# Kernel tuning notes

Hardware: AMD Instinct MI355X
Metric: run time of the kernel (lower is better)

## Reference

```python
import jax, jax.numpy as jnp
import numpy as np
import math

H = 16          # n_head
N_EMBD = 1024
EPS = 1e-5      # torch LayerNorm default


def setup_inputs() -> dict:
    key = jax.random.key(0)
    ks = jax.random.split(key, 6)
    B, T, C = 2, 2048, 1024
    x = jax.random.normal(ks[0], (B, T, C), dtype=jnp.float32)
    s = 0.02  # GPT-2 style init scale keeps softmax logits sane
    Wq = jax.random.normal(ks[1], (C, N_EMBD), dtype=jnp.float32) * s
    Wk = jax.random.normal(ks[2], (C, N_EMBD), dtype=jnp.float32) * s
    Wv = jax.random.normal(ks[3], (C, N_EMBD), dtype=jnp.float32) * s
    Wo = jax.random.normal(ks[4], (N_EMBD, C), dtype=jnp.float32) * s
    return {
        "x": x,
        "Wq": Wq, "bq": jnp.zeros((N_EMBD,), jnp.float32),
        "Wk": Wk, "bk": jnp.zeros((N_EMBD,), jnp.float32),
        "Wv": Wv, "bv": jnp.zeros((N_EMBD,), jnp.float32),
        "Wo": Wo, "bo": jnp.zeros((C,), jnp.float32),
        "gamma": jnp.ones((C,), jnp.float32),
        "beta": jnp.zeros((C,), jnp.float32),
    }


def reference(x, Wq, bq, Wk, bk, Wv, bv, Wo, bo, gamma, beta):
    B, T, _ = x.shape
    Dh = N_EMBD // H
    # projections -> (B, H, T, Dh)
    def split_heads(y):
        return y.reshape(B, T, H, Dh).transpose(0, 2, 1, 3)
    q = split_heads(x @ Wq + bq)
    k = split_heads(x @ Wk + bk)
    v = split_heads(x @ Wv + bv)
    # naive causal attention: explicit (B,H,T,T) scores
    att = jnp.einsum("bhtd,bhsd->bhts", q, k) * (1.0 / math.sqrt(Dh))
    causal = jnp.tril(jnp.ones((T, T), dtype=bool))
    att = jnp.where(causal[None, None], att, -jnp.inf)
    att = jax.nn.softmax(att, axis=-1)
    o = jnp.einsum("bhts,bhsd->bhtd", att, v)
    o = o.transpose(0, 2, 1, 3).reshape(B, T, N_EMBD)
    y = o @ Wo + bo
    # LayerNorm (dropout is identity at p=0 / eval)
    mu = jnp.mean(y, axis=-1, keepdims=True)
    var = jnp.var(y, axis=-1, keepdims=True)
    return (y - mu) * jax.lax.rsqrt(var + EPS) * gamma + beta
```

## Files before the change

### kernel.cpp

```cpp
#include <hip/hip_runtime.h>
#include <stdint.h>
#include <stddef.h>

typedef __attribute__((ext_vector_type(8))) short short8;
typedef __attribute__((ext_vector_type(4))) float f32x4;
typedef __attribute__((ext_vector_type(16))) float f32x16;
typedef __attribute__((ext_vector_type(4))) unsigned short us4;
typedef __attribute__((ext_vector_type(4))) unsigned u32x4;

#define DEVI static __device__ __forceinline__

DEVI unsigned short f2bf(float f) {
  unsigned u = __builtin_bit_cast(unsigned, f);
  u += 0x7FFFu + ((u >> 16) & 1u);
  return (unsigned short)(u >> 16);
}

DEVI float bf2f(unsigned short u) {
  return __builtin_bit_cast(float, ((unsigned)u) << 16);
}

DEVI f32x4 mfma16(short8 a, short8 b, f32x4 c) {
  return __builtin_amdgcn_mfma_f32_16x16x32_bf16(a, b, c, 0, 0, 0);
}

DEVI f32x16 mfma32(short8 a, short8 b, f32x16 c) {
  return __builtin_amdgcn_mfma_f32_32x32x16_bf16(a, b, c, 0, 0, 0);
}

DEVI unsigned cvtpk(float lo, float hi) {
  unsigned r;
  asm("v_cvt_pk_bf16_f32 %0, %1, %2" : "=v"(r) : "v"(lo), "v"(hi));
  return r;
}

DEVI void plswap(unsigned& a, unsigned& b) {
  asm("v_permlane32_swap_b32 %0, %1" : "+v"(a), "+v"(b));
}

DEVI float ex2(float x) {
  float r;
  asm("v_exp_f32 %0, %1" : "=v"(r) : "v"(x));
  return r;
}

DEVI f32x16 zero16() {
  f32x16 z;
#pragma unroll
  for (int i = 0; i < 16; ++i) z[i] = 0.f;
  return z;
}

DEVI void glds16(const void* g, void* l) {
  __builtin_amdgcn_global_load_lds(
      (const __attribute__((address_space(1))) void*)g,
      (__attribute__((address_space(3))) void*)l, 16, 0, 0);
}

__global__ __launch_bounds__(256) void k_prep(const float* __restrict__ x,
                                              unsigned short* __restrict__ xb,
                                              const float* __restrict__ W0,
                                              const float* __restrict__ W1,
                                              const float* __restrict__ W2,
                                              const float* __restrict__ W3,
                                              unsigned short* __restrict__ WT) {
  __shared__ float tile[64][65];
  const int b = blockIdx.x;
  if (b < 2048) {
    size_t i = ((size_t)b * 256 + threadIdx.x) * 8;
    f32x4 a = *(const f32x4*)(x + i);
    f32x4 v2 = *(const f32x4*)(x + i + 4);
    short8 v;
#pragma unroll
    for (int j = 0; j < 4; ++j) {
      v[j] = (short)f2bf(a[j]);
      v[4 + j] = (short)f2bf(v2[j]);
    }
    *(short8*)(xb + i) = v;
    return;
  }
  const int lin = b - 2048;
  const int z = lin >> 8, rem = lin & 255;
  const float* W = (z == 0) ? W0 : (z == 1) ? W1 : (z == 2) ? W2 : W3;
  unsigned short* out = WT + (size_t)z * 1024 * 1024;
  const int n0 = (rem & 15) * 64, k0 = (rem >> 4) * 64;
  const int t = threadIdx.x, rr = t >> 4, cc = (t & 15) * 4;
#pragma unroll
  for (int i = 0; i < 4; ++i) {
    int row = i * 16 + rr;
    f32x4 v = *(const f32x4*)(W + (size_t)(k0 + row) * 1024 + n0 + cc);
#pragma unroll
    for (int j = 0; j < 4; ++j) tile[row][cc + j] = v[j];
  }
  __syncthreads();
#pragma unroll
  for (int i = 0; i < 4; ++i) {
    int nrow = i * 16 + rr;
    us4 u;
#pragma unroll
    for (int j = 0; j < 4; ++j) u[j] = f2bf(tile[cc + j][nrow]);
    *(us4*)(out + (size_t)(n0 + nrow) * 1024 + k0 + cc) = u;
  }
}

template <bool SWAP>
DEVI void gemm_core2(const unsigned short* __restrict__ A,
                     const unsigned short* __restrict__ Bt,
                     int mt, int nt, char* lds, f32x4 (&acc)[4][4]) {
  const int t = threadIdx.x;
  const int l = t & 63, c = l & 15, g = l >> 4;
  const int w = t >> 6, wr = w >> 1, wc = w & 1;
  const int srow = t >> 3;
  const int sxor = (((t & 7) ^ (srow & 7))) * 8;
  const unsigned short* Ab = A + (size_t)(mt * 128 + srow) * 1024 + sxor;
  const unsigned short* Bb = Bt + (size_t)(nt * 128 + srow) * 1024 + sxor;
  const int key = (c & 7);

  auto STAGE = [&](int kt, int buf) {
    char* lb = lds + buf * 32768;
#pragma unroll
    for (int i = 0; i < 4; ++i) {
      glds16(Ab + (size_t)i * 32 * 1024 + kt * 64, lb + i * 4096 + t * 16);
      glds16(Bb + (size_t)i * 32 * 1024 + kt * 64, lb + 16384 + i * 4096 + t * 16);
    }
  };

  STAGE(0, 0);
  asm volatile("s_waitcnt vmcnt(0)" ::: "memory");
  __builtin_amdgcn_s_barrier();
  asm volatile("" ::: "memory");
  for (int kt = 0; kt < 16; ++kt) {
    const int cur = kt & 1;
    if (kt < 15) STAGE(kt + 1, cur ^ 1);
    const char* lb = lds + cur * 32768;
#pragma unroll
    for (int ks = 0; ks < 2; ++ks) {
      short8 af[4], bfr[4];
#pragma unroll
      for (int m = 0; m < 4; ++m)
        af[m] = *(const short8*)(lb + (wr * 64 + m * 16 + c) * 128 +
                                 ((ks * 4 + g) ^ key) * 16);
#pragma unroll
      for (int n = 0; n < 4; ++n)
        bfr[n] = *(const short8*)(lb + 16384 + (wc * 64 + n * 16 + c) * 128 +
                                  ((ks * 4 + g) ^ key) * 16);
#pragma unroll
      for (int m = 0; m < 4; ++m)
#pragma unroll
        for (int n = 0; n < 4; ++n)
          acc[m][n] = SWAP ? mfma16(bfr[n], af[m], acc[m][n])
                           : mfma16(af[m], bfr[n], acc[m][n]);
    }
    asm volatile("s_waitcnt vmcnt(0)" ::: "memory");
    __builtin_amdgcn_s_barrier();
    asm volatile("" ::: "memory");
  }
}

DEVI void gemm_core5(const unsigned short* __restrict__ A,
                     const unsigned short* __restrict__ Bt,
                     int mt, int pt, char* lds, f32x4 (&acc)[8][3]) {
  const int t = threadIdx.x;
  const int l = t & 63, c = l & 15, g = l >> 4;
  const int w = t >> 6, wm = w >> 2, wn = w & 3;
  const int srow = t >> 3;
  const int sxor = ((t & 7) ^ (srow & 7)) * 8;
  const unsigned short* Ab = A + (size_t)(mt * 256 + srow) * 1024 + sxor;
  const unsigned short* Bb = Bt + (size_t)(pt * 192 + srow) * 1024 + sxor;
  const int key = c & 7;

  auto STAGE = [&](int kt, int buf) {
    char* lb = lds + buf * 57344;
#pragma unroll
    for (int i = 0; i < 4; ++i)
      glds16(Ab + (size_t)(i * 64) * 1024 + kt * 64, lb + i * 8192 + t * 16);
#pragma unroll
    for (int i = 0; i < 3; ++i)
      glds16(Bb + (size_t)(i * 64) * 1024 + kt * 64, lb + 32768 + i * 8192 + t * 16);
  };

  STAGE(0, 0);
  asm volatile("s_waitcnt vmcnt(0)" ::: "memory");
  __builtin_amdgcn_s_barrier();
  asm volatile("" ::: "memory");
  for (int kt = 0; kt < 16; ++kt) {
    const int cur = kt & 1;
    if (kt < 15) STAGE(kt + 1, cur ^ 1);
    const char* la = lds + cur * 57344;
    const char* lbB = la + 32768;
    short8 bf[3][2];
#pragma unroll
    for (int fc = 0; fc < 3; ++fc)
#pragma unroll
      for (int ks = 0; ks < 2; ++ks) {
        int brow = wn * 48 + fc * 16 + c;
        bf[fc][ks] = *(const short8*)(lbB + brow * 128 + (((ks * 4 + g) ^ key) * 16));
      }
#pragma unroll
    for (int p = 0; p < 4; ++p) {
      short8 af[2][2];
#pragma unroll
      for (int r2 = 0; r2 < 2; ++r2)
#pragma unroll
        for (int ks = 0; ks < 2; ++ks) {
          int arow = wm * 128 + (2 * p + r2) * 16 + c;
          af[r2][ks] = *(const short8*)(la + arow * 128 + (((ks * 4 + g) ^ key) * 16));
        }
      __builtin_amdgcn_s_setprio(1);
#pragma unroll
      for (int ks = 0; ks < 2; ++ks)
#pragma unroll
        for (int r2 = 0; r2 < 2; ++r2)
#pragma unroll
          for (int fc = 0; fc < 3; ++fc)
            acc[2 * p + r2][fc] = mfma16(bf[fc][ks], af[r2][ks], acc[2 * p + r2][fc]);
      __builtin_amdgcn_s_setprio(0);
    }
    asm volatile("s_waitcnt vmcnt(0)" ::: "memory");
    __builtin_amdgcn_s_barrier();
    asm volatile("" ::: "memory");
  }
}

__global__ __launch_bounds__(512) void k_gemm_qkv3(
    const unsigned short* __restrict__ A,
    const unsigned short* __restrict__ Wf,
    const float* __restrict__ b0, const float* __restrict__ b1, const float* __restrict__ b2,
    unsigned short* __restrict__ O0, unsigned short* __restrict__ O1,
    unsigned short* __restrict__ O2) {
  extern __shared__ char lds[];
  const int mt = blockIdx.x, pt = blockIdx.y;
  f32x4 acc[8][3];
#pragma unroll
  for (int m = 0; m < 8; ++m)
#pragma unroll
    for (int n = 0; n < 3; ++n) acc[m][n] = (f32x4){0.f, 0.f, 0.f, 0.f};
  gemm_core5(A, Wf, mt, pt, lds, acc);
  const int t = threadIdx.x, l = t & 63, c = l & 15, g = l >> 4;
  const int w = t >> 6, wm = w >> 2, wn = w & 3;
#pragma unroll
  for (int fc = 0; fc < 3; ++fc) {
    int colg3 = pt * 192 + wn * 48 + fc * 16 + 4 * g;
    int z = colg3 >> 10, colc = colg3 & 1023;
    const float* bias = (z == 0) ? b0 : (z == 1) ? b1 : b2;
    f32x4 bv4 = *(const f32x4*)(bias + colc);
    int h = colc >> 6, d = colc & 63;
    if (z < 2) {
      unsigned short* out = (z == 0) ? O0 : O1;
      const float sc = (z == 0) ? 0.18033688011f : 1.0f;
#pragma unroll
      for (int fr = 0; fr < 8; ++fr) {
        int rowg = mt * 256 + wm * 128 + fr * 16 + c;
        int b = rowg >> 11, tt = rowg & 2047;
        us4 u;
#pragma unroll
        for (int r = 0; r < 4; ++r) u[r] = f2bf((acc[fr][fc][r] + bv4[r]) * sc);
        *(us4*)(out + ((size_t)(b * 16 + h) * 2048 + tt) * 64 + d) = u;
      }
    } else {
#pragma unroll
      for (int fr = 0; fr < 8; ++fr) {
        int rowg = mt * 256 + wm * 128 + fr * 16 + c;
        int b = rowg >> 11, tt = rowg & 2047;
        size_t base = ((size_t)(b * 16 + h) * 64 + d) * 2048 + tt;
#pragma unroll
        for (int r = 0; r < 4; ++r)
          O2[base + (size_t)r * 2048] = f2bf(acc[fr][fc][r] + bv4[r]);
      }
    }
  }
}

__global__ __launch_bounds__(256) void k_gemm_proj(const unsigned short* __restrict__ A,
                                                   const unsigned short* __restrict__ Bt,
                                                   const float* __restrict__ bias,
                                                   unsigned short* __restrict__ Yb) {
  __shared__ char lds[65536];
  f32x4 acc[4][4];
#pragma unroll
  for (int m = 0; m < 4; ++m)
#pragma unroll
    for (int n = 0; n < 4; ++n) acc[m][n] = (f32x4){0.f, 0.f, 0.f, 0.f};
  const int lin = blockIdx.y * 32 + blockIdx.x;
  const int nt = lin & 7, mt = lin >> 3;
  gemm_core2<true>(A, Bt, mt, nt, lds, acc);
  const int t = threadIdx.x, l = t & 63, c = l & 15, g = l >> 4;
  const int w = t >> 6, wr = w >> 1, wc = w & 1;
#pragma unroll
  for (int n = 0; n < 4; ++n) {
    int colb = nt * 128 + wc * 64 + n * 16 + 4 * g;
    f32x4 bv4 = *(const f32x4*)(bias + colb);
#pragma unroll
    for (int m = 0; m < 4; ++m) {
      int rowg = mt * 128 + wr * 64 + m * 16 + c;
      us4 u;
#pragma unroll
      for (int r = 0; r < 4; ++r) u[r] = f2bf(acc[m][n][r] + bv4[r]);
      *(us4*)(Yb + (size_t)rowg * 1024 + colb) = u;
    }
  }
}

__global__ __launch_bounds__(256) void k_attn11(const unsigned short* __restrict__ Q,
                                                const unsigned short* __restrict__ K,
                                                const unsigned short* __restrict__ VT,
                                                unsigned short* __restrict__ O,
                                                unsigned short* __restrict__ P,
                                                float* __restrict__ L) {
  __shared__ char lds[32768];
  const int bid = blockIdx.x;
  int qt, c0, NT, mode, bh, ci = 0;
  if (bid < 256) {
    int g = bid >> 5, q2 = g >> 1;
    bh = bid & 31;
    if ((g & 1) == 0) { mode = 0; qt = 7 - q2;  c0 = 0;  NT = 2 * qt + 2; }
    else              { mode = 1; qt = 15 - q2; c0 = 16; NT = 2 * qt - 14; ci = 2; }
  } else if (bid < 768) {
    int i = bid - 256, idx = i >> 5;
    bh = i & 31;
    mode = 1; qt = 8 + (idx >> 1); ci = idx & 1; c0 = ci * 8; NT = 8;
  } else {
    int i = bid - 768, g = i >> 5, q2 = g >> 1;
    bh = i & 31;
    if ((g & 1) == 0) { mode = 0; qt = 3 - q2;  c0 = 0;  NT = 2 * qt + 2; }
    else              { mode = 1; qt = 11 - q2; c0 = 16; NT = 2 * qt - 14; ci = 2; }
  }
  const int t = threadIdx.x;
  const int w = t >> 6, l = t & 63;
  const int lq = l & 31, hi = l >> 5;
  const int q0 = qt * 128 + w * 32;
  const size_t kbase = (size_t)bh * 2048 * 64;
  const size_t vbase = (size_t)bh * 64 * 2048;
  const int srow = t >> 3;
  const int sx = ((t & 7) ^ (srow & 7)) * 8;
  const bool nomask = (mode == 1 && ci < 2);
  const int my_nt = nomask ? NT : (2 * qt + 1 + (w >> 1) - c0);

  short8 qf[4];
#pragma unroll
  for (int ds = 0; ds < 4; ++ds)
    qf[ds] = *(const short8*)(Q + kbase + (size_t)(q0 + lq) * 64 + 16 * ds + 8 * hi);

  auto STAGE = [&](int ktg, int buf) {
    const unsigned short* Kt = K + kbase + (size_t)ktg * 4096;
    const unsigned short* Vt = VT + vbase + ktg * 64;
    char* lb = lds + buf * 16384;
#pragma unroll
    for (int i = 0; i < 2; ++i) {
      int row = i * 32 + srow;
      glds16(Kt + (size_t)row * 64 + sx, lb + i * 4096 + t * 16);
      glds16(Vt + (size_t)row * 2048 + sx, lb + 8192 + i * 4096 + t * 16);
    }
  };

  f32x16 oacc[2];
  oacc[0] = zero16();
  oacc[1] = zero16();
  float l_s = 0.f;
  const int rx = lq & 7;

  STAGE(c0, 0);
  for (int kt = 0; kt < NT; ++kt) {
    asm volatile("s_waitcnt vmcnt(0)" ::: "memory");
    __builtin_amdgcn_s_barrier();
    asm volatile("" ::: "memory");
    if (kt + 1 < NT) STAGE(c0 + kt + 1, (kt + 1) & 1);
    if (kt < my_nt) {
      const char* lb = lds + (kt & 1) * 16384;
      const int kv0 = (c0 + kt) * 64;
      short8 kf0[4], kf1[4];
#pragma unroll
      for (int ds = 0; ds < 4; ++ds) {
        int blk = ((ds * 2 + hi) ^ rx) * 16;
        kf0[ds] = *(const short8*)(lb + lq * 128 + blk);
        kf1[ds] = *(const short8*)(lb + (lq + 32) * 128 + blk);
      }
      f32x16 st0 = zero16(), st1 = zero16();
      __builtin_amdgcn_s_setprio(1);
#pragma unroll
      for (int ds = 0; ds < 4; ++ds) {
        st0 = mfma32(kf0[ds], qf[ds], st0);
        st1 = mfma32(kf1[ds], qf[ds], st1);
      }
      __builtin_amdgcn_s_setprio(0);
      short8 vf[2][4];
#pragma unroll
      for (int fd = 0; fd < 2; ++fd) {
        int d = fd * 32 + lq;
#pragma unroll
        for (int s = 0; s < 4; ++s)
          vf[fd][s] = *(const short8*)(lb + 8192 + d * 128 + (((s * 2 + hi) ^ rx) * 16));
      }
      if (!nomask && kt == my_nt - 1) {
        const int qg = q0 + lq;
#pragma unroll
        for (int r = 0; r < 16; ++r) {
          int kr = kv0 + (r & 3) + 8 * (r >> 2) + 4 * hi;
          if (kr > qg) st0[r] = -1e30f;
          if (kr + 32 > qg) st1[r] = -1e30f;
        }
      }
      unsigned Wp[2][4][2];
      float gs[8];
#pragma unroll
      for (int f = 0; f < 2; ++f)
#pragma unroll
        for (int m4 = 0; m4 < 4; ++m4) {
          float p0 = ex2((f ? st1 : st0)[4 * m4 + 0]);
          float p1 = ex2((f ? st1 : st0)[4 * m4 + 1]);
          float p2 = ex2((f ? st1 : st0)[4 * m4 + 2]);
          float p3 = ex2((f ? st1 : st0)[4 * m4 + 3]);
          gs[f * 4 + m4] = (p0 + p1) + (p2 + p3);
          Wp[f][m4][0] = cvtpk(p0, p1);
          Wp[f][m4][1] = cvtpk(p2, p3);
        }
      l_s += ((gs[0] + gs[1]) + (gs[2] + gs[3])) + ((gs[4] + gs[5]) + (gs[6] + gs[7]));
      __builtin_amdgcn_s_setprio(1);
#pragma unroll
      for (int s = 0; s < 4; ++s) {
        const int f = s >> 1, s2 = s & 1;
        unsigned a0 = Wp[f][2 * s2][0], b0 = Wp[f][2 * s2 + 1][0];
        unsigned a1 = Wp[f][2 * s2][1], b1 = Wp[f][2 * s2 + 1][1];
        plswap(a0, b0);
        plswap(a1, b1);
        u32x4 pw = {a0, a1, b0, b1};
        short8 pf = __builtin_bit_cast(short8, pw);
        oacc[0] = mfma32(vf[0][s], pf, oacc[0]);
        oacc[1] = mfma32(vf[1][s], pf, oacc[1]);
      }
      __builtin_amdgcn_s_setprio(0);
    }
  }
  l_s += __shfl_xor(l_s, 32, 64);
  if (mode == 0) {
    const float inv = 1.0f / l_s;
    const int b = bh >> 4, h = bh & 15;
    unsigned short* orow = O + ((size_t)b * 2048 + q0 + lq) * 1024 + h * 64 + 4 * hi;
#pragma unroll
    for (int f = 0; f < 2; ++f)
#pragma unroll
      for (int m4 = 0; m4 < 4; ++m4) {
        us4 u;
#pragma unroll
        for (int rr = 0; rr < 4; ++rr) u[rr] = f2bf(oacc[f][4 * m4 + rr] * inv);
        *(us4*)(orow + f * 32 + m4 * 8) = u;
      }
  } else {
    const int pid = ((qt - 8) * 32 + bh) * 3 + ci;
    const int row = w * 32 + lq;
    unsigned short* prow = P + (size_t)pid * 8192 + row * 64 + 4 * hi;
#pragma unroll
    for (int f = 0; f < 2; ++f)
#pragma unroll
      for (int m4 = 0; m4 < 4; ++m4) {
        us4 u;
#pragma unroll
        for (int rr = 0; rr < 4; ++rr) u[rr] = f2bf(oacc[f][4 * m4 + rr]);
        *(us4*)(prow + f * 32 + m4 * 8) = u;
      }
    if (hi == 0) L[pid * 128 + row] = l_s;
  }
}

__global__ __launch_bounds__(128) void k_merge3(const unsigned short* __restrict__ P,
                                                const float* __restrict__ L,
                                                unsigned short* __restrict__ O) {
  const int blk = blockIdx.x;
  const int qt = 8 + (blk >> 5), bh = blk & 31;
  const int pid0 = ((qt - 8) * 32 + bh) * 3;
  const int r = threadIdx.x;
  float inv = 1.f / (L[pid0 * 128 + r] + L[(pid0 + 1) * 128 + r] +
                     L[(pid0 + 2) * 128 + r]);
  const unsigned short* pa = P + (size_t)pid0 * 8192 + r * 64;
  const int b = bh >> 4, h = bh & 15, q = qt * 128 + r;
  unsigned short* orow = O + ((size_t)b * 2048 + q) * 1024 + h * 64;
#pragma unroll
  for (int j = 0; j < 8; ++j) {
    short8 a = *(const short8*)(pa + j * 8);
    short8 c = *(const short8*)(pa + 8192 + j * 8);
    short8 e = *(const short8*)(pa + 16384 + j * 8);
    short8 o;
#pragma unroll
    for (int k = 0; k < 8; ++k)
      o[k] = (short)f2bf((bf2f((unsigned short)a[k]) + bf2f((unsigned short)c[k]) +
                          bf2f((unsigned short)e[k])) * inv);
    *(short8*)(orow + j * 8) = o;
  }
}

__global__ __launch_bounds__(256) void k_ln(const unsigned short* __restrict__ Yb,
                                            const float* __restrict__ gamma,
                                            const float* __restrict__ beta,
                                            float* __restrict__ out) {
  __shared__ float red[8];
  const int row = blockIdx.x, t = threadIdx.x, w = t >> 6, l = t & 63;
  us4 vb = *(const us4*)(Yb + (size_t)row * 1024 + t * 4);
  f32x4 v;
#pragma unroll
  for (int j = 0; j < 4; ++j) v[j] = bf2f(vb[j]);
  float s = v[0] + v[1] + v[2] + v[3];
  float ss = v[0] * v[0] + v[1] * v[1] + v[2] * v[2] + v[3] * v[3];
#pragma unroll
  for (int d = 1; d < 64; d <<= 1) {
    s += __shfl_xor(s, d, 64);
    ss += __shfl_xor(ss, d, 64);
  }
  if (l == 0) {
    red[w] = s;
    red[4 + w] = ss;
  }
  __syncthreads();
  s = red[0] + red[1] + red[2] + red[3];
  ss = red[4] + red[5] + red[6] + red[7];
  float mean = s * (1.f / 1024.f);
  float var = ss * (1.f / 1024.f) - mean * mean;
  float rstd = rsqrtf(var + 1e-5f);
  f32x4 gv = *(const f32x4*)(gamma + t * 4);
  f32x4 bv = *(const f32x4*)(beta + t * 4);
  f32x4 ov;
#pragma unroll
  for (int j = 0; j < 4; ++j) ov[j] = (v[j] - mean) * rstd * gv[j] + bv[j];
  *(f32x4*)(out + (size_t)row * 1024 + t * 4) = ov;
}

extern "C" void kernel_launch(void* const* d_in, const int* in_sizes, int n_in,
                              void* d_out, int out_size, void* d_ws, size_t ws_size,
                              hipStream_t stream) {
  (void)in_sizes; (void)n_in; (void)out_size; (void)ws_size;
  const float* x = (const float*)d_in[0];
  const float* Wq = (const float*)d_in[1];
  const float* bq = (const float*)d_in[2];
  const float* Wk = (const float*)d_in[3];
  const float* bk = (const float*)d_in[4];
  const float* Wv = (const float*)d_in[5];
  const float* bv = (const float*)d_in[6];
  const float* Wo = (const float*)d_in[7];
  const float* bo = (const float*)d_in[8];
  const float* gamma = (const float*)d_in[9];
  const float* beta = (const float*)d_in[10];
  char* ws = (char*)d_ws;
  const size_t MB = 1024 * 1024;
  unsigned short* xb = (unsigned short*)(ws);
  unsigned short* WT = (unsigned short*)(ws + 8 * MB);
  unsigned short* WoT = (unsigned short*)(ws + 14 * MB);
  unsigned short* Qb = (unsigned short*)(ws + 16 * MB);
  unsigned short* Kb = (unsigned short*)(ws + 24 * MB);
  unsigned short* VTb = (unsigned short*)(ws + 32 * MB);
  unsigned short* Ob = (unsigned short*)(ws + 40 * MB);
  unsigned short* Yb = (unsigned short*)(ws + 16 * MB);
  unsigned short* Pp = (unsigned short*)(ws);
  float* Lp = (float*)(ws + 12 * MB);

  k_prep<<<3072, 256, 0, stream>>>(x, xb, Wq, Wk, Wv, Wo, WT);
  k_gemm_qkv3<<<dim3(16, 16), 512, 114688, stream>>>(xb, WT, bq, bk, bv, Qb, Kb, VTb);
  k_attn11<<<1024, 256, 0, stream>>>(Qb, Kb, VTb, Ob, Pp, Lp);
  k_merge3<<<256, 128, 0, stream>>>(Pp, Lp, Ob);
  k_gemm_proj<<<dim3(32, 8), 256, 0, stream>>>(Ob, WoT, bo, Yb);
  k_ln<<<4096, 256, 0, stream>>>(Yb, gamma, beta, (float*)d_out);
}
```

Measured before the change: 103.7 us.

## Software-pipeline attention PV matmul one tile behind QK matmul

The P·V MFMAs for the previous key tile now run right after the current tile's QK^T MFMAs. The softmax probabilities and V fragments are carried across loop iterations in registers, with a drain step after the loop. The aim is to overlap the exp/convert work with matrix-core work and cut dependency stalls between the QK, softmax and PV phases. In exchange, register pressure goes up from keeping the P and V fragments alive. An extra lgkmcnt wait is added before the barrier. If a wave runs no active tiles, the drain step uses uninitialized fragments.

```diff
diff --git a/kernel.cpp b/kernel.cpp
--- a/kernel.cpp
+++ b/kernel.cpp
@@ -301,7 +301,7 @@
   }
 }
 
-__global__ __launch_bounds__(256) void k_attn11(const unsigned short* __restrict__ Q,
+__global__ __launch_bounds__(256) void k_attn12(const unsigned short* __restrict__ Q,
                                                 const unsigned short* __restrict__ K,
                                                 const unsigned short* __restrict__ VT,
                                                 unsigned short* __restrict__ O,
@@ -358,9 +358,13 @@
   oacc[1] = zero16();
   float l_s = 0.f;
   const int rx = lq & 7;
+  unsigned WpA[2][4][2];
+  short8 vfA[2][4];
+  bool havePrev = false;
 
   STAGE(c0, 0);
   for (int kt = 0; kt < NT; ++kt) {
+    asm volatile("s_waitcnt lgkmcnt(0)" ::: "memory");
     asm volatile("s_waitcnt vmcnt(0)" ::: "memory");
     __builtin_amdgcn_s_barrier();
     asm volatile("" ::: "memory");
@@ -382,14 +386,27 @@
         st0 = mfma32(kf0[ds], qf[ds], st0);
         st1 = mfma32(kf1[ds], qf[ds], st1);
       }
+      if (havePrev) {
+#pragma unroll
+        for (int s = 0; s < 4; ++s) {
+          const int f = s >> 1, s2 = s & 1;
+          unsigned a0 = WpA[f][2 * s2][0], b0 = WpA[f][2 * s2 + 1][0];
+          unsigned a1 = WpA[f][2 * s2][1], b1 = WpA[f][2 * s2 + 1][1];
+          plswap(a0, b0);
+          plswap(a1, b1);
+          u32x4 pw = {a0, a1, b0, b1};
+          short8 pf = __builtin_bit_cast(short8, pw);
+          oacc[0] = mfma32(vfA[0][s], pf, oacc[0]);
+          oacc[1] = mfma32(vfA[1][s], pf, oacc[1]);
+        }
+      }
       __builtin_amdgcn_s_setprio(0);
-      short8 vf[2][4];
 #pragma unroll
       for (int fd = 0; fd < 2; ++fd) {
         int d = fd * 32 + lq;
 #pragma unroll
         for (int s = 0; s < 4; ++s)
-          vf[fd][s] = *(const short8*)(lb + 8192 + d * 128 + (((s * 2 + hi) ^ rx) * 16));
+          vfA[fd][s] = *(const short8*)(lb + 8192 + d * 128 + (((s * 2 + hi) ^ rx) * 16));
       }
       if (!nomask && kt == my_nt - 1) {
         const int qg = q0 + lq;
@@ -400,7 +417,6 @@
           if (kr + 32 > qg) st1[r] = -1e30f;
         }
       }
-      unsigned Wp[2][4][2];
       float gs[8];
 #pragma unroll
       for (int f = 0; f < 2; ++f)
@@ -411,25 +427,28 @@
           float p2 = ex2((f ? st1 : st0)[4 * m4 + 2]);
           float p3 = ex2((f ? st1 : st0)[4 * m4 + 3]);
           gs[f * 4 + m4] = (p0 + p1) + (p2 + p3);
-          Wp[f][m4][0] = cvtpk(p0, p1);
-          Wp[f][m4][1] = cvtpk(p2, p3);
+          WpA[f][m4][0] = cvtpk(p0, p1);
+          WpA[f][m4][1] = cvtpk(p2, p3);
         }
       l_s += ((gs[0] + gs[1]) + (gs[2] + gs[3])) + ((gs[4] + gs[5]) + (gs[6] + gs[7]));
-      __builtin_amdgcn_s_setprio(1);
-#pragma unroll
-      for (int s = 0; s < 4; ++s) {
-        const int f = s >> 1, s2 = s & 1;
-        unsigned a0 = Wp[f][2 * s2][0], b0 = Wp[f][2 * s2 + 1][0];
-        unsigned a1 = Wp[f][2 * s2][1], b1 = Wp[f][2 * s2 + 1][1];
-        plswap(a0, b0);
-        plswap(a1, b1);
-        u32x4 pw = {a0, a1, b0, b1};
-        short8 pf = __builtin_bit_cast(short8, pw);
-        oacc[0] = mfma32(vf[0][s], pf, oacc[0]);
-        oacc[1] = mfma32(vf[1][s], pf, oacc[1]);
-      }
-      __builtin_amdgcn_s_setprio(0);
-    }
+      havePrev = true;
+    }
+  }
+  {
+    __builtin_amdgcn_s_setprio(1);
+#pragma unroll
+    for (int s = 0; s < 4; ++s) {
+      const int f = s >> 1, s2 = s & 1;
+      unsigned a0 = WpA[f][2 * s2][0], b0 = WpA[f][2 * s2 + 1][0];
+      unsigned a1 = WpA[f][2 * s2][1], b1 = WpA[f][2 * s2 + 1][1];
+      plswap(a0, b0);
+      plswap(a1, b1);
+      u32x4 pw = {a0, a1, b0, b1};
+      short8 pf = __builtin_bit_cast(short8, pw);
+      oacc[0] = mfma32(vfA[0][s], pf, oacc[0]);
+      oacc[1] = mfma32(vfA[1][s], pf, oacc[1]);
+    }
+    __builtin_amdgcn_s_setprio(0);
   }
   l_s += __shfl_xor(l_s, 32, 64);
   if (mode == 0) {
@@ -553,7 +572,7 @@
 
   k_prep<<<3072, 256, 0, stream>>>(x, xb, Wq, Wk, Wv, Wo, WT);
   k_gemm_qkv3<<<dim3(16, 16), 512, 114688, stream>>>(xb, WT, bq, bk, bv, Qb, Kb, VTb);
-  k_attn11<<<1024, 256, 0, stream>>>(Qb, Kb, VTb, Ob, Pp, Lp);
+  k_attn12<<<1024, 256, 0, stream>>>(Qb, Kb, VTb, Ob, Pp, Lp);
   k_merge3<<<256, 128, 0, stream>>>(Pp, Lp, Ob);
   k_gemm_proj<<<dim3(32, 8), 256, 0, stream>>>(Ob, WoT, bo, Yb);
   k_ln<<<4096, 256, 0, stream>>>(Yb, gamma, beta, (float*)d_out);
```

Measured after the change: 102.1 us. About the same (-1.5%).
